# Kernel tuning notes

Hardware: AMD Instinct MI355X
Metric: run time of the kernel (lower is better)

## Reference

```python
import jax, jax.numpy as jnp
import numpy as np

N = 50000   # nodes
E = 600000  # edges
D = 128     # in/out features


def setup_inputs() -> dict:
    key = jax.random.key(0)
    k1, k2, k3, k4, k5, k6 = jax.random.split(key, 6)
    input = jax.random.normal(k1, (N, D), dtype=jnp.float32)
    W = jax.random.normal(k2, (D, D), dtype=jnp.float32) * (1.0 / np.sqrt(D))
    b = jax.random.normal(k3, (D,), dtype=jnp.float32) * 0.01
    adj_row = jnp.sort(jax.random.randint(k4, (E,), 0, N, dtype=jnp.int32))
    adj_col = jax.random.randint(k5, (E,), 0, N, dtype=jnp.int32)
    adj_val = jax.random.uniform(k6, (E,), dtype=jnp.float32)
    return {"input": input, "W": W, "b": b,
            "adj_row": adj_row, "adj_col": adj_col, "adj_val": adj_val}


def reference(input, W, b, adj_row, adj_col, adj_val):
    # support = Linear(input)  -> [N, D]
    support = jnp.einsum('nd,od->no', input, W) + b
    # sparse adj (COO) @ support : gather source rows, scale by edge value,
    # scatter-add into destination rows.
    msgs = support[adj_col] * adj_val[:, None]           # [E, D]
    agg = jax.ops.segment_sum(msgs, adj_row, num_segments=input.shape[0])
    return jnp.tanh(agg)
```

## Files before the change

### kernel.cpp

```cpp
#include <hip/hip_runtime.h>
#include <hip/hip_fp16.h>
#include <cmath>

#define DF 128
#define WPITCHH 136

typedef _Float16 f16x8 __attribute__((ext_vector_type(8)));
typedef _Float16 f16x4 __attribute__((ext_vector_type(4)));
typedef float    f32x4 __attribute__((ext_vector_type(4)));

__global__ __launch_bounds__(256)
void gemm_meta_kernel(const float* __restrict__ X, const float* __restrict__ W,
                      const float* __restrict__ bias, __half* __restrict__ S,
                      const int* __restrict__ arow, int* __restrict__ rowptr,
                      int N, int E, int GB)
{
    __shared__ _Float16 Wl[DF * WPITCHH];

    const int t = threadIdx.x;

    if (blockIdx.x >= GB) {
        int e = (blockIdx.x - GB) * 256 + t;
        if (e >= E) return;
        int r = arow[e];
        int rprev = (e == 0) ? -1 : arow[e - 1];
        for (int n = rprev + 1; n <= r; ++n) rowptr[n] = e;
        if (e == E - 1) {
            for (int n = r + 1; n <= N; ++n) rowptr[n] = E;
        }
        return;
    }

    const int lane = t & 63;
    const int l15  = lane & 15;
    const int q    = lane >> 4;
    const int m0   = (blockIdx.x * 4 + (t >> 6)) * 16;

    #pragma unroll
    for (int l = 0; l < 8; ++l) {
        int flat = l * 256 + t;
        int r    = flat >> 4;
        int c8   = (flat & 15) * 8;
        const float* wp = W + (size_t)r * DF + c8;
        float4 wa = *(const float4*)wp;
        float4 wb = *(const float4*)(wp + 4);
        f16x8 v;
        v[0] = (_Float16)wa.x; v[1] = (_Float16)wa.y;
        v[2] = (_Float16)wa.z; v[3] = (_Float16)wa.w;
        v[4] = (_Float16)wb.x; v[5] = (_Float16)wb.y;
        v[6] = (_Float16)wb.z; v[7] = (_Float16)wb.w;
        *(f16x8*)(Wl + r * WPITCHH + c8) = v;
    }
    __syncthreads();
    if (m0 >= N) return;

    f32x4 acc[8];
    #pragma unroll
    for (int nt = 0; nt < 8; ++nt) acc[nt] = (f32x4){0.f, 0.f, 0.f, 0.f};

    const int xrow = min(m0 + l15, N - 1);
    #pragma unroll
    for (int kc = 0; kc < DF; kc += 32) {
        const float* xp = X + (size_t)xrow * DF + kc + q * 8;
        float4 xa = *(const float4*)xp;
        float4 xb = *(const float4*)(xp + 4);
        f16x8 A;
        A[0] = (_Float16)xa.x; A[1] = (_Float16)xa.y;
        A[2] = (_Float16)xa.z; A[3] = (_Float16)xa.w;
        A[4] = (_Float16)xb.x; A[5] = (_Float16)xb.y;
        A[6] = (_Float16)xb.z; A[7] = (_Float16)xb.w;
        #pragma unroll
        for (int nt = 0; nt < 8; ++nt) {
            f16x8 B = *(const f16x8*)(Wl + (nt * 16 + l15) * WPITCHH + kc + q * 8);
            acc[nt] = __builtin_amdgcn_mfma_f32_16x16x32_f16(B, A, acc[nt], 0, 0, 0);
        }
    }

    const int mrow = m0 + l15;
    if (mrow < N) {
        _Float16* rowp = (_Float16*)S + (size_t)mrow * DF;
        #pragma unroll
        for (int nt = 0; nt < 8; ++nt) {
            float4 bv = *(const float4*)(bias + nt * 16 + q * 4);
            f16x4 hv;
            hv[0] = (_Float16)(acc[nt][0] + bv.x);
            hv[1] = (_Float16)(acc[nt][1] + bv.y);
            hv[2] = (_Float16)(acc[nt][2] + bv.z);
            hv[3] = (_Float16)(acc[nt][3] + bv.w);
            *(f16x4*)(rowp + nt * 16 + q * 4) = hv;
        }
    }
}

__global__ __launch_bounds__(256)
void build_epk_kernel(const int* __restrict__ arow, const int* __restrict__ acol,
                      const float* __restrict__ aval, const int* __restrict__ rowptr,
                      int2* __restrict__ epk, int N, int E)
{
    int tid = blockIdx.x * 256 + threadIdx.x;
    if (tid < E) {
        int n    = arow[tid];
        int base = rowptr[n];
        int s2   = (base + 8 * n + 7) & ~7;
        epk[s2 + (tid - base)] = make_int2(acol[tid] << 8, __float_as_int(aval[tid]));
    }
    if (tid < N) {
        int start = rowptr[tid];
        int end   = rowptr[tid + 1];
        int cnt   = end - start;
        int s2    = (start + 8 * tid + 7) & ~7;
        int cpad  = (cnt + 7) & ~7;
        for (int k = cnt; k < cpad; ++k) epk[s2 + k] = make_int2(0, 0);
    }
}

__global__ __launch_bounds__(256)
void agg_tanh_kernel(const __half* __restrict__ S, const int* __restrict__ rowptr,
                     const int2* __restrict__ epk, float* __restrict__ out, int Nn)
{
    const int n  = (blockIdx.x * 256 + threadIdx.x) >> 4;
    if (n >= Nn) return;
    const int f  = threadIdx.x & 15;
    const int fb = f * 16;

    const int start = rowptr[n];
    const int cnt   = rowptr[n + 1] - start;
    const int s2    = (start + 8 * n + 7) & ~7;
    const char* Sb  = (const char*)S;

    float acc[8];
    #pragma unroll
    for (int i = 0; i < 8; ++i) acc[i] = 0.f;

    for (int b = 0; b < cnt; b += 8) {
        const int2* pp = epk + s2 + b;
        int2 p[8];
        #pragma unroll
        for (int u = 0; u < 8; ++u) p[u] = pp[u];
        f16x8 h[8];
        #pragma unroll
        for (int u = 0; u < 8; ++u)
            h[u] = *(const f16x8*)(Sb + (size_t)(unsigned)p[u].x + fb);
        #pragma unroll
        for (int u = 0; u < 8; ++u) {
            const float v = __int_as_float(p[u].y);
            #pragma unroll
            for (int i = 0; i < 8; ++i) acc[i] += (float)h[u][i] * v;
        }
    }

    float4 o0, o1;
    o0.x = tanhf(acc[0]); o0.y = tanhf(acc[1]);
    o0.z = tanhf(acc[2]); o0.w = tanhf(acc[3]);
    o1.x = tanhf(acc[4]); o1.y = tanhf(acc[5]);
    o1.z = tanhf(acc[6]); o1.w = tanhf(acc[7]);
    float* op = out + (size_t)n * DF + f * 8;
    *(float4*)op       = o0;
    *(float4*)(op + 4) = o1;
}

extern "C" void kernel_launch(void* const* d_in, const int* in_sizes, int n_in,
                              void* d_out, int out_size, void* d_ws, size_t ws_size,
                              hipStream_t stream)
{
    const float* X    = (const float*)d_in[0];
    const float* W    = (const float*)d_in[1];
    const float* bias = (const float*)d_in[2];
    const int*   arow = (const int*)  d_in[3];
    const int*   acol = (const int*)  d_in[4];
    const float* aval = (const float*)d_in[5];
    float* out = (float*)d_out;

    const int N = in_sizes[0] / DF;
    const int E = in_sizes[3];

    __half* S      = (__half*)d_ws;
    int*    rowptr = (int*)((char*)d_ws + (size_t)N * DF * sizeof(__half));
    int2*   epk    = (int2*)(rowptr + (N + 2));

    const int GB = (N + 63) / 64;
    const int MB = (E + 255) / 256;

    gemm_meta_kernel<<<GB + MB, 256, 0, stream>>>(X, W, bias, S, arow, rowptr,
                                                  N, E, GB);

    build_epk_kernel<<<(E + 255) / 256, 256, 0, stream>>>(arow, acol, aval,
                                                          rowptr, epk, N, E);

    agg_tanh_kernel<<<(N * 16 + 255) / 256, 256, 0, stream>>>(S, rowptr, epk, out, N);
}
```

Baseline: 125.4 us.

## Split support matrix into four feature-quarter planes for cache-local gather

The GEMM now writes the fp16 support matrix as four separate planes of 32 features each, not as one row-major 128-wide array. Each aggregation block handles one quarter, so the random gathers for that block fall within a 3.2 MB plane that fits better in L2/LLC. Blocks are interleaved so the four quarters of a pair of node chunks are scheduled close together. In exchange, the edge list and rowptr are read four times, and per-row gather segments shrink to 64 bytes.

```diff
diff --git a/kernel.cpp b/kernel.cpp
--- a/kernel.cpp
+++ b/kernel.cpp
@@ -3,6 +3,7 @@
 #include <cmath>
 
 #define DF 128
+#define QF 32
 #define WPITCHH 136
 
 typedef _Float16 f16x8 __attribute__((ext_vector_type(8)));
@@ -11,7 +12,7 @@
 
 __global__ __launch_bounds__(256)
 void gemm_meta_kernel(const float* __restrict__ X, const float* __restrict__ W,
-                      const float* __restrict__ bias, __half* __restrict__ S,
+                      const float* __restrict__ bias, _Float16* __restrict__ S4,
                       const int* __restrict__ arow, int* __restrict__ rowptr,
                       int N, int E, int GB)
 {
@@ -33,7 +34,7 @@
 
     const int lane = t & 63;
     const int l15  = lane & 15;
-    const int q    = lane >> 4;
+    const int q4   = lane >> 4;
     const int m0   = (blockIdx.x * 4 + (t >> 6)) * 16;
 
     #pragma unroll
@@ -61,7 +62,7 @@
     const int xrow = min(m0 + l15, N - 1);
     #pragma unroll
     for (int kc = 0; kc < DF; kc += 32) {
-        const float* xp = X + (size_t)xrow * DF + kc + q * 8;
+        const float* xp = X + (size_t)xrow * DF + kc + q4 * 8;
         float4 xa = *(const float4*)xp;
         float4 xb = *(const float4*)(xp + 4);
         f16x8 A;
@@ -71,23 +72,24 @@
         A[6] = (_Float16)xb.z; A[7] = (_Float16)xb.w;
         #pragma unroll
         for (int nt = 0; nt < 8; ++nt) {
-            f16x8 B = *(const f16x8*)(Wl + (nt * 16 + l15) * WPITCHH + kc + q * 8);
+            f16x8 B = *(const f16x8*)(Wl + (nt * 16 + l15) * WPITCHH + kc + q4 * 8);
             acc[nt] = __builtin_amdgcn_mfma_f32_16x16x32_f16(B, A, acc[nt], 0, 0, 0);
         }
     }
 
     const int mrow = m0 + l15;
     if (mrow < N) {
-        _Float16* rowp = (_Float16*)S + (size_t)mrow * DF;
         #pragma unroll
         for (int nt = 0; nt < 8; ++nt) {
-            float4 bv = *(const float4*)(bias + nt * 16 + q * 4);
+            float4 bv = *(const float4*)(bias + nt * 16 + q4 * 4);
             f16x4 hv;
             hv[0] = (_Float16)(acc[nt][0] + bv.x);
             hv[1] = (_Float16)(acc[nt][1] + bv.y);
             hv[2] = (_Float16)(acc[nt][2] + bv.z);
             hv[3] = (_Float16)(acc[nt][3] + bv.w);
-            *(f16x4*)(rowp + nt * 16 + q * 4) = hv;
+            _Float16* dst = S4 + (size_t)(nt >> 1) * N * QF
+                               + (size_t)mrow * QF + (nt & 1) * 16 + q4 * 4;
+            *(f16x4*)dst = hv;
         }
     }
 }
@@ -102,7 +104,7 @@
         int n    = arow[tid];
         int base = rowptr[n];
         int s2   = (base + 8 * n + 7) & ~7;
-        epk[s2 + (tid - base)] = make_int2(acol[tid] << 8, __float_as_int(aval[tid]));
+        epk[s2 + (tid - base)] = make_int2(acol[tid] << 6, __float_as_int(aval[tid]));
     }
     if (tid < N) {
         int start = rowptr[tid];
@@ -115,25 +117,28 @@
 }
 
 __global__ __launch_bounds__(256)
-void agg_tanh_kernel(const __half* __restrict__ S, const int* __restrict__ rowptr,
+void agg_tanh_kernel(const _Float16* __restrict__ S4, const int* __restrict__ rowptr,
                      const int2* __restrict__ epk, float* __restrict__ out, int Nn)
 {
-    const int n  = (blockIdx.x * 256 + threadIdx.x) >> 4;
+    const int b     = blockIdx.x;
+    const int q     = (b & 7) >> 1;
+    const int chunk = (b >> 3) * 2 + (b & 1);
+    const int n     = chunk * 64 + (threadIdx.x >> 2);
     if (n >= Nn) return;
-    const int f  = threadIdx.x & 15;
+    const int f  = threadIdx.x & 3;
     const int fb = f * 16;
 
     const int start = rowptr[n];
     const int cnt   = rowptr[n + 1] - start;
     const int s2    = (start + 8 * n + 7) & ~7;
-    const char* Sb  = (const char*)S;
+    const char* Sb  = (const char*)(S4 + (size_t)q * Nn * QF);
 
     float acc[8];
     #pragma unroll
     for (int i = 0; i < 8; ++i) acc[i] = 0.f;
 
-    for (int b = 0; b < cnt; b += 8) {
-        const int2* pp = epk + s2 + b;
+    for (int bb = 0; bb < cnt; bb += 8) {
+        const int2* pp = epk + s2 + bb;
         int2 p[8];
         #pragma unroll
         for (int u = 0; u < 8; ++u) p[u] = pp[u];
@@ -154,7 +159,7 @@
     o0.z = tanhf(acc[2]); o0.w = tanhf(acc[3]);
     o1.x = tanhf(acc[4]); o1.y = tanhf(acc[5]);
     o1.z = tanhf(acc[6]); o1.w = tanhf(acc[7]);
-    float* op = out + (size_t)n * DF + f * 8;
+    float* op = out + (size_t)n * DF + q * QF + f * 8;
     *(float4*)op       = o0;
     *(float4*)(op + 4) = o1;
 }
@@ -174,18 +179,19 @@
     const int N = in_sizes[0] / DF;
     const int E = in_sizes[3];
 
-    __half* S      = (__half*)d_ws;
-    int*    rowptr = (int*)((char*)d_ws + (size_t)N * DF * sizeof(__half));
-    int2*   epk    = (int2*)(rowptr + (N + 2));
+    _Float16* S4     = (_Float16*)d_ws;
+    int*      rowptr = (int*)((char*)d_ws + (size_t)N * DF * sizeof(_Float16));
+    int2*     epk    = (int2*)(rowptr + (N + 2));
 
     const int GB = (N + 63) / 64;
     const int MB = (E + 255) / 256;
 
-    gemm_meta_kernel<<<GB + MB, 256, 0, stream>>>(X, W, bias, S, arow, rowptr,
+    gemm_meta_kernel<<<GB + MB, 256, 0, stream>>>(X, W, bias, S4, arow, rowptr,
                                                   N, E, GB);
 
     build_epk_kernel<<<(E + 255) / 256, 256, 0, stream>>>(arow, acol, aval,
                                                           rowptr, epk, N, E);
 
-    agg_tanh_kernel<<<(N * 16 + 255) / 256, 256, 0, stream>>>(S, rowptr, epk, out, N);
+    const int GBe = (((N + 63) / 64) + 1) & ~1;
+    agg_tanh_kernel<<<GBe * 4, 256, 0, stream>>>(S4, rowptr, epk, out, N);
 }
```

Result: slower. 128.0 us (+2.1%).
